# Performance work log

Measured on AMD Instinct MI355X. Metric: run time of the kernel, lower is better.

## Reference

```python
import jax, jax.numpy as jnp
import numpy as np

B, S, D = 2, 4096, 256
H, KD = 8, 256  # keras MHA built with key_dim=d_model -> per-head dim = 256
DFF = 1024
EPS = 1e-3  # keras LayerNormalization default epsilon
NEG = 1e9


def setup_inputs() -> dict:
    key = jax.random.key(0)
    ks = jax.random.split(key, 16)
    sd = 0.02
    return {
        "x": jax.random.normal(ks[0], (B, S, D), jnp.float32),
        "w_2": 128,
        "Wq": jax.random.normal(ks[1], (D, H, KD), jnp.float32) * sd,
        "bq": jnp.zeros((H, KD), jnp.float32),
        "Wk": jax.random.normal(ks[2], (D, H, KD), jnp.float32) * sd,
        "bk": jnp.zeros((H, KD), jnp.float32),
        "Wv": jax.random.normal(ks[3], (D, H, KD), jnp.float32) * sd,
        "bv": jnp.zeros((H, KD), jnp.float32),
        "Wo": jax.random.normal(ks[4], (H, KD, D), jnp.float32) * sd,
        "bo": jnp.zeros((D,), jnp.float32),
        "W1": jax.random.normal(ks[5], (D, DFF), jnp.float32) * sd,
        "b1": jnp.zeros((DFF,), jnp.float32),
        "W2": jax.random.normal(ks[6], (DFF, D), jnp.float32) * sd,
        "b2": jnp.zeros((D,), jnp.float32),
        "g1": jnp.ones((D,), jnp.float32),
        "be1": jnp.zeros((D,), jnp.float32),
        "g2": jnp.ones((D,), jnp.float32),
        "be2": jnp.zeros((D,), jnp.float32),
    }


def layer_norm(x, g, b):
    mu = jnp.mean(x, axis=-1, keepdims=True)
    var = jnp.mean(jnp.square(x - mu), axis=-1, keepdims=True)
    return (x - mu) * jax.lax.rsqrt(var + EPS) * g + b


def reference(x, w_2, Wq, bq, Wk, bk, Wv, bv, Wo, bo, W1, b1, W2, b2, g1, be1, g2, be2):
    # --- sliding-window self attention (dense scores + mask, as in source) ---
    q = jnp.einsum('bsd,dhk->bshk', x, Wq) + bq
    k = jnp.einsum('bsd,dhk->bshk', x, Wk) + bk
    v = jnp.einsum('bsd,dhk->bshk', x, Wv) + bv
    scores = jnp.einsum('bqhd,bkhd->bhqk', q, k) / jnp.sqrt(jnp.asarray(KD, x.dtype))
    idx = jnp.arange(S)
    mask = (jnp.abs(idx[:, None] - idx[None, :]) <= w_2)  # [S, S]
    scores = scores + (1.0 - mask.astype(x.dtype)) * (-NEG)
    attn = jax.nn.softmax(scores, axis=-1)
    ctx = jnp.einsum('bhqk,bkhd->bqhd', attn, v)
    attn_out = jnp.einsum('bqhd,hdo->bqo', ctx, Wo) + bo
    x = layer_norm(x + attn_out, g1, be1)
    # --- feed-forward ---
    h = jax.nn.relu(jnp.einsum('bsd,df->bsf', x, W1) + b1)
    ffn = jnp.einsum('bsf,fd->bsd', h, W2) + b2
    x = layer_norm(x + ffn, g2, be2)
    return x
```

## Files before the change

kernel.cpp:

```cpp
#include <hip/hip_runtime.h>
#include <hip/hip_bf16.h>

#define Bn 2
#define Sn 4096
#define Dn 256
#define Hn 8
#define KDn 256
#define DFFn 1024
#define Mn (Bn*Sn)
#define NQKVn (Hn*KDn)

typedef __attribute__((ext_vector_type(4))) float f32x4;
typedef __attribute__((ext_vector_type(8))) short bf16x8;
typedef __attribute__((ext_vector_type(4))) short short4v;

__device__ __forceinline__ short f2bf(float f) {
  unsigned u = __builtin_bit_cast(unsigned, f);
  unsigned r = u + 0x7fffu + ((u >> 16) & 1u);
  return (short)(r >> 16);
}

#define GLL16(gsrc, ldst) \
  __builtin_amdgcn_global_load_lds((const __attribute__((address_space(1))) void*)(gsrc), \
                                   (__attribute__((address_space(3))) void*)(ldst), 16, 0, 0)

#define WAITCNT4 asm volatile("s_waitcnt vmcnt(4)" ::: "memory")
#define WAITCNT2 asm volatile("s_waitcnt vmcnt(2)" ::: "memory")
#define WAITCNT0 asm volatile("s_waitcnt vmcnt(0)" ::: "memory")
#define BARRIER  do { __builtin_amdgcn_s_barrier(); asm volatile("" ::: "memory"); } while (0)

__global__ __launch_bounds__(256)
void cvt_x(const float* __restrict__ x, short* __restrict__ xb, int n) {
  int i = (blockIdx.x * 256 + threadIdx.x) * 4;
  if (i < n) {
    float4 v = *(const float4*)(x + i);
    short4v o = { f2bf(v.x), f2bf(v.y), f2bf(v.z), f2bf(v.w) };
    *(short4v*)(xb + i) = o;
  }
}

__global__ __launch_bounds__(256)
void concat_bias(const float* __restrict__ bq, const float* __restrict__ bk,
                 const float* __restrict__ bv, float* __restrict__ o) {
  int i = blockIdx.x * 256 + threadIdx.x;
  o[i] = (i < 2048) ? bq[i] : (i < 4096 ? bk[i - 2048] : bv[i - 4096]);
}

__global__ __launch_bounds__(256)
void cvt_weights(const float* __restrict__ Wq, const float* __restrict__ Wk,
                 const float* __restrict__ Wv, const float* __restrict__ Wo,
                 const float* __restrict__ W1, const float* __restrict__ W2,
                 short* __restrict__ WqT, short* __restrict__ WkT,
                 short* __restrict__ WvT, short* __restrict__ WoT,
                 short* __restrict__ W1T, short* __restrict__ W2T) {
  int t = blockIdx.x;
  const float* W; short* WT; int K, N;
  if      (t < 512)  { W = Wq; WT = WqT; K = 256;  N = 2048; }
  else if (t < 1024) { t -= 512;  W = Wk; WT = WkT; K = 256;  N = 2048; }
  else if (t < 1536) { t -= 1024; W = Wv; WT = WvT; K = 256;  N = 2048; }
  else if (t < 2048) { t -= 1536; W = Wo; WT = WoT; K = 2048; N = 256;  }
  else if (t < 2304) { t -= 2048; W = W1; WT = W1T; K = 256;  N = 1024; }
  else               { t -= 2304; W = W2; WT = W2T; K = 1024; N = 256;  }
  const int ktiles = K >> 5;
  const int k0 = (t % ktiles) * 32, n0 = (t / ktiles) * 32;
  __shared__ short tt[32][33];
  const int tx = threadIdx.x & 31, ty = threadIdx.x >> 5;
#pragma unroll
  for (int i = 0; i < 32; i += 8)
    tt[ty + i][tx] = f2bf(W[(size_t)(k0 + ty + i) * N + n0 + tx]);
  __syncthreads();
#pragma unroll
  for (int i = 0; i < 32; i += 8)
    WT[(size_t)(n0 + ty + i) * K + k0 + tx] = tt[tx][ty + i];
}

__global__ __launch_bounds__(256, 3)
void gemm_qkv(const short* __restrict__ A, const short* __restrict__ BT,
              const float* __restrict__ bias, short* __restrict__ Qo,
              short* __restrict__ Ko, short* __restrict__ Vto) {
  __shared__ __align__(16) short smem[3 * 8192];
  const int tid = threadIdx.x;
  const int lane = tid & 63;
  const int wave = tid >> 6;
  const int tn = blockIdx.x;
  const int tm = blockIdx.y;
  const int wr = (wave >> 1) * 64;
  const int wc = (wave & 1) * 64;
  const int lrow = lane & 15;
  const int lk = (lane >> 4) * 8;

  f32x4 acc[4][4];
#pragma unroll
  for (int i = 0; i < 4; ++i)
#pragma unroll
    for (int j = 0; j < 4; ++j) acc[i][j] = (f32x4){0.f, 0.f, 0.f, 0.f};

  const int row_s = tid >> 2;
  const int col_s = (tid & 3) * 8;
  const short* aB = A + (size_t)(tm * 128 + row_s) * 256 + col_s;
  const short* bB = BT + (size_t)(tn * 128 + row_s) * 256 + col_s;

  auto stage = [&](int kt, int bf) {
    const short* aP = aB + kt * 32;
    const short* bP = bB + kt * 32;
    short* AsB = smem + bf * 8192 + wave * 512;
    short* BsB = smem + bf * 8192 + 4096 + wave * 512;
    GLL16(aP, AsB);
    GLL16(aP + 64 * 256, AsB + 2048);
    GLL16(bP, BsB);
    GLL16(bP + 64 * 256, BsB + 2048);
  };

  stage(0, 0);
  stage(1, 1);
  int cur = 0;
  for (int kt = 0; kt < 8; ++kt) {
    if (kt == 7) WAITCNT0; else WAITCNT4;
    BARRIER;
    if (kt + 2 < 8) { int nb = cur + 2; if (nb >= 3) nb -= 3; stage(kt + 2, nb); }
    const short* As = smem + cur * 8192;
    const short* Bs = As + 4096;
    bf16x8 af[4], bfr[4];
#pragma unroll
    for (int i = 0; i < 4; ++i) {
      af[i]  = *(const bf16x8*)(As + (wr + i * 16 + lrow) * 32 + lk);
      bfr[i] = *(const bf16x8*)(Bs + (wc + i * 16 + lrow) * 32 + lk);
    }
#pragma unroll
    for (int i = 0; i < 4; ++i)
#pragma unroll
      for (int j = 0; j < 4; ++j)
        acc[i][j] = __builtin_amdgcn_mfma_f32_16x16x32_bf16(af[i], bfr[j], acc[i][j], 0, 0, 0);
    ++cur; if (cur == 3) cur = 0;
  }

  const int rbase = (lane >> 4) * 4;
  if (tn < 32) {
    short* C = (tn < 16) ? Qo : Ko;
    const float sc = (tn < 16) ? 1.f : 0.0625f;
    const int cb = (tn & 15) * 128;
#pragma unroll
    for (int j = 0; j < 4; ++j) {
      const int cj = wc + j * 16 + lrow;
      const float bv = bias[tn * 128 + cj];
      const int cl = cb + cj;
#pragma unroll
      for (int i = 0; i < 4; ++i) {
        const int row0 = tm * 128 + wr + i * 16 + rbase;
        f32x4 a = acc[i][j];
#pragma unroll
        for (int r = 0; r < 4; ++r)
          C[(size_t)(row0 + r) * NQKVn + cl] = f2bf((a[r] + bv) * sc);
      }
    }
  } else {
    __syncthreads();
    short* Ct = smem;
#pragma unroll
    for (int j = 0; j < 4; ++j) {
      const int colL = wc + j * 16 + lrow;
      const float bv = bias[tn * 128 + colL];
#pragma unroll
      for (int i = 0; i < 4; ++i) {
        const int rowL0 = wr + i * 16 + rbase;
        f32x4 a = acc[i][j];
        short4v o = { f2bf(a[0] + bv), f2bf(a[1] + bv), f2bf(a[2] + bv), f2bf(a[3] + bv) };
        *(short4v*)(&Ct[colL * 130 + rowL0]) = o;
      }
    }
    __syncthreads();
    const int kd_l = tid >> 1;
    const int so = (tid & 1) * 64;
    const int cl = (tn - 32) * 128 + kd_l;
    const int hh = cl >> 8;
    const int kd = cl & 255;
    const int row0 = tm * 128;
    const int bb = row0 >> 12;
    const int s0 = (row0 & (Sn - 1)) + so;
    short* dst = Vto + (size_t)((bb * Hn + hh) * KDn + kd) * Sn + s0;
#pragma unroll
    for (int u = 0; u < 64; u += 8)
      *(bf16x8*)(dst + u) = *(const bf16x8*)(&Ct[kd_l * 130 + so + u]);
  }
}

__global__ __launch_bounds__(256, 3)
void gemm_ffn1(const short* __restrict__ A, const short* __restrict__ BT,
               const float* __restrict__ bias, short* __restrict__ C,
               int N, int K) {
  __shared__ __align__(16) short smem[3 * 8192];
  const int tid = threadIdx.x;
  const int lane = tid & 63;
  const int wave = tid >> 6;
  const int tn = blockIdx.x;
  const int tm = blockIdx.y;
  const int wr = (wave >> 1) * 64;
  const int wc = (wave & 1) * 64;
  const int lrow = lane & 15;
  const int lk = (lane >> 4) * 8;

  f32x4 acc[4][4];
#pragma unroll
  for (int i = 0; i < 4; ++i)
#pragma unroll
    for (int j = 0; j < 4; ++j) acc[i][j] = (f32x4){0.f, 0.f, 0.f, 0.f};

  const int row_s = tid >> 2;
  const int col_s = (tid & 3) * 8;
  const short* aB = A + (size_t)(tm * 128 + row_s) * K + col_s;
  const short* bB = BT + (size_t)(tn * 128 + row_s) * K + col_s;

  auto stage = [&](int kt, int bf) {
    const short* aP = aB + kt * 32;
    const short* bP = bB + kt * 32;
    short* AsB = smem + bf * 8192 + wave * 512;
    short* BsB = smem + bf * 8192 + 4096 + wave * 512;
    GLL16(aP, AsB);
    GLL16(aP + (size_t)64 * K, AsB + 2048);
    GLL16(bP, BsB);
    GLL16(bP + (size_t)64 * K, BsB + 2048);
  };

  const int nk = K >> 5;
  stage(0, 0);
  if (nk > 1) stage(1, 1);
  int cur = 0;
  for (int kt = 0; kt < nk; ++kt) {
    if (kt == nk - 1) WAITCNT0; else WAITCNT4;
    BARRIER;
    if (kt + 2 < nk) { int nb = cur + 2; if (nb >= 3) nb -= 3; stage(kt + 2, nb); }
    const short* As = smem + cur * 8192;
    const short* Bs = As + 4096;
    bf16x8 af[4], bfr[4];
#pragma unroll
    for (int i = 0; i < 4; ++i) {
      af[i]  = *(const bf16x8*)(As + (wr + i * 16 + lrow) * 32 + lk);
      bfr[i] = *(const bf16x8*)(Bs + (wc + i * 16 + lrow) * 32 + lk);
    }
#pragma unroll
    for (int i = 0; i < 4; ++i)
#pragma unroll
      for (int j = 0; j < 4; ++j)
        acc[i][j] = __builtin_amdgcn_mfma_f32_16x16x32_bf16(af[i], bfr[j], acc[i][j], 0, 0, 0);
    ++cur; if (cur == 3) cur = 0;
  }

  const int rbase = (lane >> 4) * 4;
#pragma unroll
  for (int j = 0; j < 4; ++j) {
    const int col = tn * 128 + wc + j * 16 + lrow;
    const float bv = bias[col];
#pragma unroll
    for (int i = 0; i < 4; ++i) {
      const int row0 = tm * 128 + wr + i * 16 + rbase;
      f32x4 a = acc[i][j];
#pragma unroll
      for (int r = 0; r < 4; ++r)
        C[(size_t)(row0 + r) * N + col] = f2bf(fmaxf(a[r] + bv, 0.f));
    }
  }
}

__global__ __launch_bounds__(256, 4)
void gemm_bt64(const short* __restrict__ A, const short* __restrict__ BT,
               const float* __restrict__ bias, float* __restrict__ C,
               int N, int K) {
  __shared__ __align__(16) short smem[3 * 4096];
  const int tid = threadIdx.x;
  const int lane = tid & 63;
  const int wave = tid >> 6;
  const int tn = blockIdx.x;
  const int tm = blockIdx.y;
  const int wr = (wave >> 1) * 32;
  const int wc = (wave & 1) * 32;
  const int lrow = lane & 15;
  const int lk = (lane >> 4) * 8;

  f32x4 acc[2][2];
#pragma unroll
  for (int i = 0; i < 2; ++i)
#pragma unroll
    for (int j = 0; j < 2; ++j) acc[i][j] = (f32x4){0.f, 0.f, 0.f, 0.f};

  const int row_s = tid >> 2;
  const int col_s = (tid & 3) * 8;
  const short* aB = A + (size_t)(tm * 64 + row_s) * K + col_s;
  const short* bB = BT + (size_t)(tn * 64 + row_s) * K + col_s;

  auto stage = [&](int kt, int bf) {
    GLL16(aB + kt * 32, smem + bf * 4096 + wave * 512);
    GLL16(bB + kt * 32, smem + bf * 4096 + 2048 + wave * 512);
  };

  const int nk = K >> 5;
  stage(0, 0);
  if (nk > 1) stage(1, 1);
  int cur = 0;
  for (int kt = 0; kt < nk; ++kt) {
    if (kt == nk - 1) WAITCNT0; else WAITCNT2;
    BARRIER;
    if (kt + 2 < nk) { int nb = cur + 2; if (nb >= 3) nb -= 3; stage(kt + 2, nb); }
    const short* As = smem + cur * 4096;
    const short* Bs = As + 2048;
    bf16x8 af[2], bfr[2];
#pragma unroll
    for (int i = 0; i < 2; ++i) {
      af[i]  = *(const bf16x8*)(As + (wr + i * 16 + lrow) * 32 + lk);
      bfr[i] = *(const bf16x8*)(Bs + (wc + i * 16 + lrow) * 32 + lk);
    }
#pragma unroll
    for (int i = 0; i < 2; ++i)
#pragma unroll
      for (int j = 0; j < 2; ++j)
        acc[i][j] = __builtin_amdgcn_mfma_f32_16x16x32_bf16(af[i], bfr[j], acc[i][j], 0, 0, 0);
    ++cur; if (cur == 3) cur = 0;
  }

  const int rbase = (lane >> 4) * 4;
#pragma unroll
  for (int j = 0; j < 2; ++j) {
    const int col = tn * 64 + wc + j * 16 + lrow;
    const float bv = bias[col];
#pragma unroll
    for (int i = 0; i < 2; ++i) {
      const int row0 = tm * 64 + wr + i * 16 + rbase;
      f32x4 a = acc[i][j];
#pragma unroll
      for (int r = 0; r < 4; ++r) C[(size_t)(row0 + r) * N + col] = a[r] + bv;
    }
  }
}

__global__ __launch_bounds__(512, 1)
void attn_win(const short* __restrict__ q, const short* __restrict__ k,
              const short* __restrict__ vt, short* __restrict__ ctx,
              const int* __restrict__ w2p) {
  const int bid = blockIdx.x;
  const int swz = (bid & 7) * 32 + (bid >> 3);
  const int q0 = (swz & 15) * 256;
  const int h = (swz >> 4) & 7;
  const int b = swz >> 7;
  const int tid = threadIdx.x;
  const int lane = tid & 63;
  const int wave = tid >> 6;
  const int w2 = *w2p;
  const int qw = q0 + wave * 32;
  const int lrow = lane & 15;
  const int lk = (lane >> 4) * 8;
  const int lk2 = lk * 2;
  const int rbase = (lane >> 4) * 4;

  __shared__ __align__(16) short Ks[3][8192];
  __shared__ __align__(16) short Vs[3][8192];
  __shared__ __align__(16) short Ps[8][1024];
  short* P = Ps[wave];

  const short* qbase = q + (size_t)(b * Sn + qw) * NQKVn + h * KDn;
  bf16x8 qf[2][8];
#pragma unroll
  for (int mi = 0; mi < 2; ++mi)
#pragma unroll
    for (int ks = 0; ks < 8; ++ks)
      qf[mi][ks] = *(const bf16x8*)(qbase + (size_t)(mi * 16 + lrow) * NQKVn + ks * 32 + lk);

  f32x4 oacc[2][16];
#pragma unroll
  for (int mi = 0; mi < 2; ++mi)
#pragma unroll
    for (int nc = 0; nc < 16; ++nc) oacc[mi][nc] = (f32x4){0.f, 0.f, 0.f, 0.f};

  float lsum[2][4];
#pragma unroll
  for (int mi = 0; mi < 2; ++mi)
#pragma unroll
    for (int r = 0; r < 4; ++r) lsum[mi][r] = 0.f;

  const short* kbase = k + (size_t)(b * Sn) * NQKVn + h * KDn;
  const short* vtb = vt + (size_t)((b * Hn + h) * KDn) * Sn;

  int bstart = q0 - w2; if (bstart < 0) bstart = 0; bstart &= ~31;
  int bend = q0 + 256 + w2; if (bend > Sn) bend = Sn; bend = (bend + 31) & ~31;
  int wlo = qw - w2; if (wlo < 0) wlo = 0; wlo &= ~31;
  int whi = qw + 32 + w2; if (whi > Sn) whi = Sn;

  auto stage = [&](int c0, int bf) {
#pragma unroll
    for (int e = 0; e < 2; ++e) {
      const int o = e * 8192 + tid * 16;
      const int row = o >> 9;
      const int cc = (o & 511) ^ ((row & 7) << 4);
      GLL16(kbase + (size_t)(c0 + row) * NQKVn + (cc >> 1),
            (char*)Ks[bf] + e * 8192 + wave * 1024);
    }
#pragma unroll
    for (int e = 0; e < 2; ++e) {
      const int o = e * 8192 + tid * 16;
      const int row = o >> 6;
      const int cc = (o & 63) ^ ((row & 3) << 4);
      GLL16(vtb + (size_t)row * Sn + c0 + (cc >> 1),
            (char*)Vs[bf] + e * 8192 + wave * 1024);
    }
  };

  const int nch = (bend - bstart) >> 5;
  stage(bstart, 0);
  if (nch > 1) stage(bstart + 32, 1);

  int cur = 0;
  for (int i = 0; i < nch; ++i) {
    const int c0 = bstart + i * 32;
    if (i == nch - 1) WAITCNT0; else WAITCNT4;
    BARRIER;
    if (i + 2 < nch) { int nb = cur + 2; if (nb >= 3) nb -= 3; stage(c0 + 64, nb); }

    if (c0 >= wlo && c0 < whi) {
      const char* Kc = (const char*)Ks[cur];
      const int x0 = (lrow & 7) << 4;
      f32x4 sf[2][2];
      sf[0][0] = sf[0][1] = sf[1][0] = sf[1][1] = (f32x4){0.f, 0.f, 0.f, 0.f};
#pragma unroll
      for (int ks = 0; ks < 8; ++ks) {
        const int cb = (lk2 + ks * 64) ^ x0;
        bf16x8 kf0 = *(const bf16x8*)(Kc + lrow * 512 + cb);
        bf16x8 kf1 = *(const bf16x8*)(Kc + (16 + lrow) * 512 + cb);
        sf[0][0] = __builtin_amdgcn_mfma_f32_16x16x32_bf16(qf[0][ks], kf0, sf[0][0], 0, 0, 0);
        sf[0][1] = __builtin_amdgcn_mfma_f32_16x16x32_bf16(qf[0][ks], kf1, sf[0][1], 0, 0, 0);
        sf[1][0] = __builtin_amdgcn_mfma_f32_16x16x32_bf16(qf[1][ks], kf0, sf[1][0], 0, 0, 0);
        sf[1][1] = __builtin_amdgcn_mfma_f32_16x16x32_bf16(qf[1][ks], kf1, sf[1][1], 0, 0, 0);
      }
      const bool full = (c0 >= qw + 31 - w2) && (c0 + 31 <= qw + w2);
      if (full) {
#pragma unroll
        for (int mi = 0; mi < 2; ++mi)
#pragma unroll
          for (int ni = 0; ni < 2; ++ni)
#pragma unroll
            for (int r = 0; r < 4; ++r) {
              const float p = __expf(sf[mi][ni][r]);
              sf[mi][ni][r] = p;
              lsum[mi][r] += p;
            }
      } else {
#pragma unroll
        for (int mi = 0; mi < 2; ++mi)
#pragma unroll
          for (int ni = 0; ni < 2; ++ni) {
            const int kk = c0 + ni * 16 + lrow;
#pragma unroll
            for (int r = 0; r < 4; ++r) {
              const int dd = (qw + mi * 16 + rbase + r) - kk;
              const bool val = (dd <= w2) && (dd >= -w2);
              float p = __expf(sf[mi][ni][r]);
              p = val ? p : 0.f;
              sf[mi][ni][r] = p;
              lsum[mi][r] += p;
            }
          }
      }
#pragma unroll
      for (int mi = 0; mi < 2; ++mi)
#pragma unroll
        for (int ni = 0; ni < 2; ++ni)
#pragma unroll
          for (int r = 0; r < 4; ++r)
            P[(mi * 16 + rbase + r) * 32 + ni * 16 + lrow] = f2bf(sf[mi][ni][r]);

      bf16x8 pa0 = *(const bf16x8*)(P + lrow * 32 + lk);
      bf16x8 pa1 = *(const bf16x8*)(P + (16 + lrow) * 32 + lk);
      const char* Vc = (const char*)Vs[cur] + lrow * 64 + (lk2 ^ ((lrow & 3) << 4));
#pragma unroll
      for (int nc = 0; nc < 16; ++nc) {
        bf16x8 vf = *(const bf16x8*)(Vc + nc * 1024);
        oacc[0][nc] = __builtin_amdgcn_mfma_f32_16x16x32_bf16(pa0, vf, oacc[0][nc], 0, 0, 0);
        oacc[1][nc] = __builtin_amdgcn_mfma_f32_16x16x32_bf16(pa1, vf, oacc[1][nc], 0, 0, 0);
      }
    }
    ++cur; if (cur == 3) cur = 0;
  }

#pragma unroll
  for (int mi = 0; mi < 2; ++mi)
#pragma unroll
    for (int r = 0; r < 4; ++r) {
      float s = lsum[mi][r];
#pragma unroll
      for (int d = 1; d < 16; d <<= 1) s += __shfl_xor(s, d);
      lsum[mi][r] = 1.f / s;
    }

  short* cbase = ctx + (size_t)(b * Sn + qw) * NQKVn + h * KDn;
#pragma unroll
  for (int mi = 0; mi < 2; ++mi)
#pragma unroll
    for (int nc = 0; nc < 16; ++nc)
#pragma unroll
      for (int r = 0; r < 4; ++r)
        cbase[(size_t)(mi * 16 + rbase + r) * NQKVn + nc * 16 + lrow] =
            f2bf(oacc[mi][nc][r] * lsum[mi][r]);
}

__global__ __launch_bounds__(256)
void ln_fused(const float* __restrict__ xin, const float* __restrict__ yin,
              const float* __restrict__ g, const float* __restrict__ bb,
              float* __restrict__ of32, short* __restrict__ obf) {
  const int row = blockIdx.x * 4 + (threadIdx.x >> 6);
  const int lane = threadIdx.x & 63;
  const size_t base = (size_t)row * Dn + lane * 4;
  float4 a = *(const float4*)(xin + base);
  float4 bv = *(const float4*)(yin + base);
  float4 v = { a.x + bv.x, a.y + bv.y, a.z + bv.z, a.w + bv.w };
  float sum = v.x + v.y + v.z + v.w;
  float ssq = v.x * v.x + v.y * v.y + v.z * v.z + v.w * v.w;
#pragma unroll
  for (int d = 1; d < 64; d <<= 1) { sum += __shfl_xor(sum, d); ssq += __shfl_xor(ssq, d); }
  const float mu = sum * (1.f / Dn);
  const float var = ssq * (1.f / Dn) - mu * mu;
  const float rs = rsqrtf(var + 1e-3f);
  float4 gg = *(const float4*)(g + lane * 4);
  float4 bbv = *(const float4*)(bb + lane * 4);
  float4 o = { (v.x - mu) * rs * gg.x + bbv.x, (v.y - mu) * rs * gg.y + bbv.y,
               (v.z - mu) * rs * gg.z + bbv.z, (v.w - mu) * rs * gg.w + bbv.w };
  if (of32) *(float4*)(of32 + base) = o;
  if (obf) {
    short4v ob = { f2bf(o.x), f2bf(o.y), f2bf(o.z), f2bf(o.w) };
    *(short4v*)(obf + base) = ob;
  }
}

extern "C" void kernel_launch(void* const* d_in, const int* in_sizes, int n_in,
                              void* d_out, int out_size, void* d_ws, size_t ws_size,
                              hipStream_t stream) {
  const float* x   = (const float*)d_in[0];
  const int*   w2p = (const int*)d_in[1];
  const float* Wq  = (const float*)d_in[2];
  const float* bq  = (const float*)d_in[3];
  const float* Wk  = (const float*)d_in[4];
  const float* bk  = (const float*)d_in[5];
  const float* Wv  = (const float*)d_in[6];
  const float* bv  = (const float*)d_in[7];
  const float* Wo  = (const float*)d_in[8];
  const float* bo  = (const float*)d_in[9];
  const float* W1  = (const float*)d_in[10];
  const float* b1  = (const float*)d_in[11];
  const float* W2  = (const float*)d_in[12];
  const float* b2  = (const float*)d_in[13];
  const float* g1  = (const float*)d_in[14];
  const float* be1 = (const float*)d_in[15];
  const float* g2  = (const float*)d_in[16];
  const float* be2 = (const float*)d_in[17];
  float* out = (float*)d_out;

  char* ws = (char*)d_ws;
  size_t off = 0;
  auto alloc = [&](size_t bytes) { void* p = ws + off; off += (bytes + 255) & ~(size_t)255; return p; };
  short* xb    = (short*)alloc((size_t)Mn * Dn * 2);
  short* WqkvT = (short*)alloc((size_t)3 * NQKVn * Dn * 2);
  float* bqkv  = (float*)alloc((size_t)3 * NQKVn * 4);
  short* WoT   = (short*)alloc((size_t)Dn * NQKVn * 2);
  short* W1T   = (short*)alloc((size_t)DFFn * Dn * 2);
  short* W2T   = (short*)alloc((size_t)Dn * DFFn * 2);
  short* qb    = (short*)alloc((size_t)Mn * NQKVn * 2);
  short* kb    = (short*)alloc((size_t)Mn * NQKVn * 2);
  short* vtb   = (short*)alloc((size_t)Mn * NQKVn * 2);
  float* attn_out = (float*)alloc((size_t)Mn * Dn * 4);
  float* x1    = (float*)alloc((size_t)Mn * Dn * 4);
  short* ctxb = qb;
  short* x1b  = xb;
  short* hb   = kb;
  float* ffn  = attn_out;

  cvt_x<<<dim3(Mn * Dn / 1024), dim3(256), 0, stream>>>(x, xb, Mn * Dn);
  cvt_weights<<<dim3(2560), dim3(256), 0, stream>>>(
      Wq, Wk, Wv, Wo, W1, W2,
      WqkvT, WqkvT + (size_t)NQKVn * Dn, WqkvT + (size_t)2 * NQKVn * Dn,
      WoT, W1T, W2T);
  concat_bias<<<dim3(24), dim3(256), 0, stream>>>(bq, bk, bv, bqkv);

  gemm_qkv<<<dim3(48, 64), dim3(256), 0, stream>>>(xb, WqkvT, bqkv, qb, kb, vtb);

  attn_win<<<dim3(256), dim3(512), 0, stream>>>(qb, kb, vtb, ctxb, w2p);

  gemm_bt64<<<dim3(Dn / 64, Mn / 64), dim3(256), 0, stream>>>(ctxb, WoT, bo, attn_out, Dn, NQKVn);
  ln_fused<<<dim3(Mn / 4), dim3(256), 0, stream>>>(x, attn_out, g1, be1, x1, x1b);
  gemm_ffn1<<<dim3(DFFn / 128, Mn / 128), dim3(256), 0, stream>>>(x1b, W1T, b1, hb, DFFn, Dn);
  gemm_bt64<<<dim3(Dn / 64, Mn / 64), dim3(256), 0, stream>>>(hb, W2T, b2, ffn, Dn, DFFn);
  ln_fused<<<dim3(Mn / 4), dim3(256), 0, stream>>>(x1, ffn, g2, be2, out, (short*)nullptr);
}
```

Measured before the change: 187.5 us.

## Fuse output-projection and FFN2 GEMMs with residual LayerNorm; tweak attention softmax

Replaces the 64x64 GEMM plus separate LayerNorm kernels with a gemm_ln kernel where each block computes 32 full rows of 256 columns. It adds bias and residual, reduces mean and variance across waves through shared memory, and writes the normalized output directly. This removes the fp32 attn_out/ffn round trips and two launches. It also uses XOR-swizzled LDS staging, raises wave priority around the MFMA loops, folds log2(e) into the K scale so softmax can use exp2f, and pads the P buffer stride to reduce bank conflicts. Fewer blocks per GEMM (256) may reduce occupancy and parallelism.

Result: slower. 207.4 us (+10.6%).

```diff
diff --git a/kernel.cpp b/kernel.cpp
--- a/kernel.cpp
+++ b/kernel.cpp
@@ -24,8 +24,8 @@
   __builtin_amdgcn_global_load_lds((const __attribute__((address_space(1))) void*)(gsrc), \
                                    (__attribute__((address_space(3))) void*)(ldst), 16, 0, 0)
 
+#define WAITCNT5 asm volatile("s_waitcnt vmcnt(5)" ::: "memory")
 #define WAITCNT4 asm volatile("s_waitcnt vmcnt(4)" ::: "memory")
-#define WAITCNT2 asm volatile("s_waitcnt vmcnt(2)" ::: "memory")
 #define WAITCNT0 asm volatile("s_waitcnt vmcnt(0)" ::: "memory")
 #define BARRIER  do { __builtin_amdgcn_s_barrier(); asm volatile("" ::: "memory"); } while (0)
 
@@ -126,18 +126,20 @@
       af[i]  = *(const bf16x8*)(As + (wr + i * 16 + lrow) * 32 + lk);
       bfr[i] = *(const bf16x8*)(Bs + (wc + i * 16 + lrow) * 32 + lk);
     }
+    __builtin_amdgcn_s_setprio(1);
 #pragma unroll
     for (int i = 0; i < 4; ++i)
 #pragma unroll
       for (int j = 0; j < 4; ++j)
         acc[i][j] = __builtin_amdgcn_mfma_f32_16x16x32_bf16(af[i], bfr[j], acc[i][j], 0, 0, 0);
+    __builtin_amdgcn_s_setprio(0);
     ++cur; if (cur == 3) cur = 0;
   }
 
   const int rbase = (lane >> 4) * 4;
   if (tn < 32) {
     short* C = (tn < 16) ? Qo : Ko;
-    const float sc = (tn < 16) ? 1.f : 0.0625f;
+    const float sc = (tn < 16) ? 1.f : (0.0625f * 1.4426950408889634f);
     const int cb = (tn & 15) * 128;
 #pragma unroll
     for (int j = 0; j < 4; ++j) {
@@ -237,11 +239,13 @@
       af[i]  = *(const bf16x8*)(As + (wr + i * 16 + lrow) * 32 + lk);
       bfr[i] = *(const bf16x8*)(Bs + (wc + i * 16 + lrow) * 32 + lk);
     }
+    __builtin_amdgcn_s_setprio(1);
 #pragma unroll
     for (int i = 0; i < 4; ++i)
 #pragma unroll
       for (int j = 0; j < 4; ++j)
         acc[i][j] = __builtin_amdgcn_mfma_f32_16x16x32_bf16(af[i], bfr[j], acc[i][j], 0, 0, 0);
+    __builtin_amdgcn_s_setprio(0);
     ++cur; if (cur == 3) cur = 0;
   }
 
@@ -261,74 +265,154 @@
   }
 }
 
-__global__ __launch_bounds__(256, 4)
-void gemm_bt64(const short* __restrict__ A, const short* __restrict__ BT,
-               const float* __restrict__ bias, float* __restrict__ C,
-               int N, int K) {
-  __shared__ __align__(16) short smem[3 * 4096];
+__global__ __launch_bounds__(256, 2)
+void gemm_ln(const short* __restrict__ A, const short* __restrict__ BT,
+             const float* __restrict__ bias, const float* __restrict__ resid,
+             const float* __restrict__ g, const float* __restrict__ be,
+             float* __restrict__ outF, short* __restrict__ outB, int K) {
+  __shared__ __align__(16) short AsL[3][1024];
+  __shared__ __align__(16) short BsL[3][8192];
+  __shared__ float red[4][32][2];
   const int tid = threadIdx.x;
   const int lane = tid & 63;
   const int wave = tid >> 6;
-  const int tn = blockIdx.x;
-  const int tm = blockIdx.y;
-  const int wr = (wave >> 1) * 32;
-  const int wc = (wave & 1) * 32;
+  const int tm = blockIdx.x;
+  const int wc = wave * 64;
   const int lrow = lane & 15;
   const int lk = (lane >> 4) * 8;
-
-  f32x4 acc[2][2];
+  const int sseg = lane >> 4;
+  const int rbase = (lane >> 4) * 4;
+  const int row0g = tm * 32;
+
+  f32x4 acc[2][4];
 #pragma unroll
   for (int i = 0; i < 2; ++i)
 #pragma unroll
-    for (int j = 0; j < 2; ++j) acc[i][j] = (f32x4){0.f, 0.f, 0.f, 0.f};
-
-  const int row_s = tid >> 2;
-  const int col_s = (tid & 3) * 8;
-  const short* aB = A + (size_t)(tm * 64 + row_s) * K + col_s;
-  const short* bB = BT + (size_t)(tn * 64 + row_s) * K + col_s;
+    for (int j = 0; j < 4; ++j) acc[i][j] = (f32x4){0.f, 0.f, 0.f, 0.f};
+
+  const int srow = tid >> 2;
+  const int sslt = tid & 3;
 
   auto stage = [&](int kt, int bf) {
-    GLL16(aB + kt * 32, smem + bf * 4096 + wave * 512);
-    GLL16(bB + kt * 32, smem + bf * 4096 + 2048 + wave * 512);
+#pragma unroll
+    for (int e = 0; e < 4; ++e) {
+      const int row = e * 64 + srow;
+      const int sP = sslt ^ ((row >> 1) & 3);
+      GLL16(BT + (size_t)row * K + kt * 32 + sP * 8,
+            (char*)BsL[bf] + e * 4096 + wave * 1024);
+    }
+    if (tid < 128) {
+      const int sP = sslt ^ ((srow >> 1) & 3);
+      GLL16(A + (size_t)(row0g + srow) * K + kt * 32 + sP * 8,
+            (char*)AsL[bf] + wave * 1024);
+    }
   };
 
   const int nk = K >> 5;
   stage(0, 0);
-  if (nk > 1) stage(1, 1);
+  stage(1, 1);
   int cur = 0;
   for (int kt = 0; kt < nk; ++kt) {
-    if (kt == nk - 1) WAITCNT0; else WAITCNT2;
+    if (kt == nk - 1) { WAITCNT0; }
+    else if (wave < 2) { WAITCNT5; }
+    else { WAITCNT4; }
     BARRIER;
     if (kt + 2 < nk) { int nb = cur + 2; if (nb >= 3) nb -= 3; stage(kt + 2, nb); }
-    const short* As = smem + cur * 4096;
-    const short* Bs = As + 2048;
-    bf16x8 af[2], bfr[2];
+    const char* Asb = (const char*)AsL[cur];
+    const char* Bsb = (const char*)BsL[cur];
+    bf16x8 af[2], bfr[4];
 #pragma unroll
     for (int i = 0; i < 2; ++i) {
-      af[i]  = *(const bf16x8*)(As + (wr + i * 16 + lrow) * 32 + lk);
-      bfr[i] = *(const bf16x8*)(Bs + (wc + i * 16 + lrow) * 32 + lk);
-    }
+      const int row = i * 16 + lrow;
+      af[i] = *(const bf16x8*)(Asb + row * 64 + ((sseg ^ ((row >> 1) & 3)) * 16));
+    }
+#pragma unroll
+    for (int j = 0; j < 4; ++j) {
+      const int row = wc + j * 16 + lrow;
+      bfr[j] = *(const bf16x8*)(Bsb + row * 64 + ((sseg ^ ((row >> 1) & 3)) * 16));
+    }
+    __builtin_amdgcn_s_setprio(1);
 #pragma unroll
     for (int i = 0; i < 2; ++i)
 #pragma unroll
-      for (int j = 0; j < 2; ++j)
+      for (int j = 0; j < 4; ++j)
         acc[i][j] = __builtin_amdgcn_mfma_f32_16x16x32_bf16(af[i], bfr[j], acc[i][j], 0, 0, 0);
+    __builtin_amdgcn_s_setprio(0);
     ++cur; if (cur == 3) cur = 0;
   }
 
-  const int rbase = (lane >> 4) * 4;
-#pragma unroll
-  for (int j = 0; j < 2; ++j) {
-    const int col = tn * 64 + wc + j * 16 + lrow;
-    const float bv = bias[col];
-#pragma unroll
-    for (int i = 0; i < 2; ++i) {
-      const int row0 = tm * 64 + wr + i * 16 + rbase;
-      f32x4 a = acc[i][j];
-#pragma unroll
-      for (int r = 0; r < 4; ++r) C[(size_t)(row0 + r) * N + col] = a[r] + bv;
-    }
-  }
+  float bcol[4];
+#pragma unroll
+  for (int j = 0; j < 4; ++j) bcol[j] = bias[wc + j * 16 + lrow];
+  float vals[2][4][4];
+  float psum[8], pssq[8];
+#pragma unroll
+  for (int t = 0; t < 8; ++t) { psum[t] = 0.f; pssq[t] = 0.f; }
+#pragma unroll
+  for (int i = 0; i < 2; ++i)
+#pragma unroll
+    for (int r = 0; r < 4; ++r) {
+      const int rowg = row0g + i * 16 + rbase + r;
+#pragma unroll
+      for (int j = 0; j < 4; ++j) {
+        const int col = wc + j * 16 + lrow;
+        const float v = acc[i][j][r] + bcol[j] + resid[(size_t)rowg * Dn + col];
+        vals[i][j][r] = v;
+        psum[i * 4 + r] += v;
+        pssq[i * 4 + r] += v * v;
+      }
+    }
+#pragma unroll
+  for (int t = 0; t < 8; ++t) {
+#pragma unroll
+    for (int d = 1; d < 16; d <<= 1) {
+      psum[t] += __shfl_xor(psum[t], d);
+      pssq[t] += __shfl_xor(pssq[t], d);
+    }
+  }
+  if (lrow == 0) {
+#pragma unroll
+    for (int i = 0; i < 2; ++i)
+#pragma unroll
+      for (int r = 0; r < 4; ++r) {
+        red[wave][i * 16 + rbase + r][0] = psum[i * 4 + r];
+        red[wave][i * 16 + rbase + r][1] = pssq[i * 4 + r];
+      }
+  }
+  __syncthreads();
+  float mu_[8], rs_[8];
+#pragma unroll
+  for (int i = 0; i < 2; ++i)
+#pragma unroll
+    for (int r = 0; r < 4; ++r) {
+      const int rowl = i * 16 + rbase + r;
+      const float s = red[0][rowl][0] + red[1][rowl][0] + red[2][rowl][0] + red[3][rowl][0];
+      const float q = red[0][rowl][1] + red[1][rowl][1] + red[2][rowl][1] + red[3][rowl][1];
+      const float mu = s * (1.f / Dn);
+      const float var = q * (1.f / Dn) - mu * mu;
+      mu_[i * 4 + r] = mu;
+      rs_[i * 4 + r] = rsqrtf(var + 1e-3f);
+    }
+  float gcol[4], becol[4];
+#pragma unroll
+  for (int j = 0; j < 4; ++j) {
+    gcol[j] = g[wc + j * 16 + lrow];
+    becol[j] = be[wc + j * 16 + lrow];
+  }
+#pragma unroll
+  for (int i = 0; i < 2; ++i)
+#pragma unroll
+    for (int r = 0; r < 4; ++r) {
+      const int rowg = row0g + i * 16 + rbase + r;
+      const float mu = mu_[i * 4 + r], rs = rs_[i * 4 + r];
+#pragma unroll
+      for (int j = 0; j < 4; ++j) {
+        const int col = wc + j * 16 + lrow;
+        const float o = (vals[i][j][r] - mu) * rs * gcol[j] + becol[j];
+        if (outF) outF[(size_t)rowg * Dn + col] = o;
+        if (outB) outB[(size_t)rowg * Dn + col] = f2bf(o);
+      }
+    }
 }
 
 __global__ __launch_bounds__(512, 1)
@@ -352,7 +436,7 @@
 
   __shared__ __align__(16) short Ks[3][8192];
   __shared__ __align__(16) short Vs[3][8192];
-  __shared__ __align__(16) short Ps[8][1024];
+  __shared__ __align__(16) short Ps[8][1280];
   short* P = Ps[wave];
 
   const short* qbase = q + (size_t)(b * Sn + qw) * NQKVn + h * KDn;
@@ -436,7 +520,7 @@
           for (int ni = 0; ni < 2; ++ni)
 #pragma unroll
             for (int r = 0; r < 4; ++r) {
-              const float p = __expf(sf[mi][ni][r]);
+              const float p = exp2f(sf[mi][ni][r]);
               sf[mi][ni][r] = p;
               lsum[mi][r] += p;
             }
@@ -450,7 +534,7 @@
             for (int r = 0; r < 4; ++r) {
               const int dd = (qw + mi * 16 + rbase + r) - kk;
               const bool val = (dd <= w2) && (dd >= -w2);
-              float p = __expf(sf[mi][ni][r]);
+              float p = exp2f(sf[mi][ni][r]);
               p = val ? p : 0.f;
               sf[mi][ni][r] = p;
               lsum[mi][r] += p;
@@ -463,10 +547,10 @@
         for (int ni = 0; ni < 2; ++ni)
 #pragma unroll
           for (int r = 0; r < 4; ++r)
-            P[(mi * 16 + rbase + r) * 32 + ni * 16 + lrow] = f2bf(sf[mi][ni][r]);
-
-      bf16x8 pa0 = *(const bf16x8*)(P + lrow * 32 + lk);
-      bf16x8 pa1 = *(const bf16x8*)(P + (16 + lrow) * 32 + lk);
+            P[(mi * 16 + rbase + r) * 40 + ni * 16 + lrow] = f2bf(sf[mi][ni][r]);
+
+      bf16x8 pa0 = *(const bf16x8*)(P + lrow * 40 + lk);
+      bf16x8 pa1 = *(const bf16x8*)(P + (16 + lrow) * 40 + lk);
       const char* Vc = (const char*)Vs[cur] + lrow * 64 + (lk2 ^ ((lrow & 3) << 4));
 #pragma unroll
       for (int nc = 0; nc < 16; ++nc) {
@@ -497,34 +581,6 @@
       for (int r = 0; r < 4; ++r)
         cbase[(size_t)(mi * 16 + rbase + r) * NQKVn + nc * 16 + lrow] =
             f2bf(oacc[mi][nc][r] * lsum[mi][r]);
-}
-
-__global__ __launch_bounds__(256)
-void ln_fused(const float* __restrict__ xin, const float* __restrict__ yin,
-              const float* __restrict__ g, const float* __restrict__ bb,
-              float* __restrict__ of32, short* __restrict__ obf) {
-  const int row = blockIdx.x * 4 + (threadIdx.x >> 6);
-  const int lane = threadIdx.x & 63;
-  const size_t base = (size_t)row * Dn + lane * 4;
-  float4 a = *(const float4*)(xin + base);
-  float4 bv = *(const float4*)(yin + base);
-  float4 v = { a.x + bv.x, a.y + bv.y, a.z + bv.z, a.w + bv.w };
-  float sum = v.x + v.y + v.z + v.w;
-  float ssq = v.x * v.x + v.y * v.y + v.z * v.z + v.w * v.w;
-#pragma unroll
-  for (int d = 1; d < 64; d <<= 1) { sum += __shfl_xor(sum, d); ssq += __shfl_xor(ssq, d); }
-  const float mu = sum * (1.f / Dn);
-  const float var = ssq * (1.f / Dn) - mu * mu;
-  const float rs = rsqrtf(var + 1e-3f);
-  float4 gg = *(const float4*)(g + lane * 4);
-  float4 bbv = *(const float4*)(bb + lane * 4);
-  float4 o = { (v.x - mu) * rs * gg.x + bbv.x, (v.y - mu) * rs * gg.y + bbv.y,
-               (v.z - mu) * rs * gg.z + bbv.z, (v.w - mu) * rs * gg.w + bbv.w };
-  if (of32) *(float4*)(of32 + base) = o;
-  if (obf) {
-    short4v ob = { f2bf(o.x), f2bf(o.y), f2bf(o.z), f2bf(o.w) };
-    *(short4v*)(obf + base) = ob;
-  }
 }
 
 extern "C" void kernel_launch(void* const* d_in, const int* in_sizes, int n_in,
@@ -562,12 +618,10 @@
   short* qb    = (short*)alloc((size_t)Mn * NQKVn * 2);
   short* kb    = (short*)alloc((size_t)Mn * NQKVn * 2);
   short* vtb   = (short*)alloc((size_t)Mn * NQKVn * 2);
-  float* attn_out = (float*)alloc((size_t)Mn * Dn * 4);
   float* x1    = (float*)alloc((size_t)Mn * Dn * 4);
   short* ctxb = qb;
   short* x1b  = xb;
   short* hb   = kb;
-  float* ffn  = attn_out;
 
   cvt_x<<<dim3(Mn * Dn / 1024), dim3(256), 0, stream>>>(x, xb, Mn * Dn);
   cvt_weights<<<dim3(2560), dim3(256), 0, stream>>>(
@@ -580,9 +634,7 @@
 
   attn_win<<<dim3(256), dim3(512), 0, stream>>>(qb, kb, vtb, ctxb, w2p);
 
-  gemm_bt64<<<dim3(Dn / 64, Mn / 64), dim3(256), 0, stream>>>(ctxb, WoT, bo, attn_out, Dn, NQKVn);
-  ln_fused<<<dim3(Mn / 4), dim3(256), 0, stream>>>(x, attn_out, g1, be1, x1, x1b);
+  gemm_ln<<<dim3(Mn / 32), dim3(256), 0, stream>>>(ctxb, WoT, bo, x, g1, be1, x1, x1b, NQKVn);
   gemm_ffn1<<<dim3(DFFn / 128, Mn / 128), dim3(256), 0, stream>>>(x1b, W1T, b1, hb, DFFn, Dn);
-  gemm_bt64<<<dim3(Dn / 64, Mn / 64), dim3(256), 0, stream>>>(hb, W2T, b2, ffn, Dn, DFFn);
-  ln_fused<<<dim3(Mn / 4), dim3(256), 0, stream>>>(x1, ffn, g2, be2, out, (short*)nullptr);
-}
+  gemm_ln<<<dim3(Mn / 32), dim3(256), 0, stream>>>(hb, W2T, b2, x1, g2, be2, out, (short*)nullptr, DFFn);
+}
```
